# Performance work log

Measured on AMD Instinct MI355X. Metric: run time of the kernel, lower is better.

## Reference

```python
import jax, jax.numpy as jnp
import numpy as np
import math

D_MODEL = 2048
N_HEADS = 32
N_KV_HEADS = 8
HEAD_DIM = D_MODEL // N_HEADS  # 64
N_GROUPS = N_HEADS // N_KV_HEADS  # 4
MAX_SEQ_LEN = 2048
ROPE_THETA = 500000.0


def precompute_rope(head_dim, max_seq_len, theta=ROPE_THETA):
    freqs = 1.0 / theta ** (jnp.arange(0, head_dim, 2, dtype=jnp.float32) / head_dim)
    positions = jnp.arange(max_seq_len, dtype=jnp.float32)
    angles = jnp.outer(positions, freqs)  # [S, head_dim/2]
    return jnp.cos(angles), jnp.sin(angles)


def apply_rope(x, cos, sin):
    # x: [B, H, S, D]; cos/sin: [S, D/2]
    half = x.shape[-1] // 2
    x1, x2 = x[..., :half], x[..., half:]
    cos = cos[None, None]
    sin = sin[None, None]
    return jnp.concatenate([x1 * cos - x2 * sin, x1 * sin + x2 * cos], axis=-1)


def setup_inputs() -> dict:
    key = jax.random.key(0)
    k1, k2, k3, k4, k5 = jax.random.split(key, 5)
    B, S = 2, 2048
    x = jax.random.normal(k1, (B, S, D_MODEL), dtype=jnp.float32)
    sd = 1.0 / math.sqrt(D_MODEL)
    # weights stored as [in, out] so forward is x @ W (same math as torch Linear)
    W_q = jax.random.normal(k2, (D_MODEL, N_HEADS * HEAD_DIM), dtype=jnp.float32) * sd
    W_k = jax.random.normal(k3, (D_MODEL, N_KV_HEADS * HEAD_DIM), dtype=jnp.float32) * sd
    W_v = jax.random.normal(k4, (D_MODEL, N_KV_HEADS * HEAD_DIM), dtype=jnp.float32) * sd
    W_o = jax.random.normal(k5, (N_HEADS * HEAD_DIM, D_MODEL), dtype=jnp.float32) * sd
    cos, sin = precompute_rope(HEAD_DIM, MAX_SEQ_LEN)
    return {"x": x, "W_q": W_q, "W_k": W_k, "W_v": W_v, "W_o": W_o,
            "rope_cos": cos, "rope_sin": sin}


def reference(x, W_q, W_k, W_v, W_o, rope_cos, rope_sin):
    B, S, _ = x.shape
    scale = 1.0 / math.sqrt(HEAD_DIM)
    # projections -> [B, H, S, D]
    q = (x @ W_q).reshape(B, S, N_HEADS, HEAD_DIM).transpose(0, 2, 1, 3)
    k = (x @ W_k).reshape(B, S, N_KV_HEADS, HEAD_DIM).transpose(0, 2, 1, 3)
    v = (x @ W_v).reshape(B, S, N_KV_HEADS, HEAD_DIM).transpose(0, 2, 1, 3)
    # RoPE
    q = apply_rope(q, rope_cos[:S], rope_sin[:S])
    k = apply_rope(k, rope_cos[:S], rope_sin[:S])
    # GQA expand: repeat each KV head n_groups times
    k = jnp.repeat(k, N_GROUPS, axis=1)  # [B, H, S, D]
    v = jnp.repeat(v, N_GROUPS, axis=1)
    # scores + causal mask + softmax
    scores = jnp.einsum('bhqd,bhkd->bhqk', q, k) * scale
    causal = jnp.tril(jnp.ones((S, S), dtype=bool))
    scores = jnp.where(causal[None, None], scores, -jnp.inf)
    weights = jax.nn.softmax(scores, axis=-1)
    attn_out = jnp.einsum('bhqk,bhkd->bhqd', weights, v)
    out = attn_out.transpose(0, 2, 1, 3).reshape(B, S, N_HEADS * HEAD_DIM) @ W_o
    return out
```

## Files before the change

kernel.cpp:

```cpp
#include <hip/hip_runtime.h>
#include <hip/hip_bf16.h>

typedef __attribute__((ext_vector_type(8))) short short8;
typedef __attribute__((ext_vector_type(4))) short short4v;
typedef __attribute__((ext_vector_type(4))) float f32x4;

#define MFMA(A,B,C) __builtin_amdgcn_mfma_f32_16x16x32_bf16(A,B,C,0,0,0)
#define SW(row) ((((row) & 3)) | (((row) >> 1) & 4))
#define SCL 0.18033688f

__device__ __forceinline__ short f2bs(float f) {
    __hip_bfloat16 h = __float2bfloat16(f);
    union { __hip_bfloat16 h; short s; } u; u.h = h; return u.s;
}

__device__ __forceinline__ float exp2v(float x) {
    float r; asm("v_exp_f32 %0, %1" : "=v"(r) : "v"(x)); return r;
}

__device__ __forceinline__ unsigned cvtpk(float a, float b) {
    unsigned r; asm("v_cvt_pk_bf16_f32 %0, %1, %2" : "=v"(r) : "v"(a), "v"(b)); return r;
}

__device__ __forceinline__ void async16(void* lds, const void* g) {
    __builtin_amdgcn_global_load_lds(
        (const __attribute__((address_space(1))) unsigned int*)g,
        (__attribute__((address_space(3))) unsigned int*)lds, 16, 0, 0);
}

__global__ __launch_bounds__(256) void cast_bf16_k(const float* __restrict__ X,
                                                   short* __restrict__ Y, int n4) {
    int i = blockIdx.x * 256 + threadIdx.x;
    if (i >= n4) return;
    const float4 v = *(const float4*)(X + (size_t)i * 4);
    short4v o;
    o.x = f2bs(v.x); o.y = f2bs(v.y); o.z = f2bs(v.z); o.w = f2bs(v.w);
    *(short4v*)(Y + (size_t)i * 4) = o;
}

__global__ __launch_bounds__(256) void transpose_cast_k(const float* __restrict__ W,
                                                        short* __restrict__ Wt, int K, int N) {
    __shared__ float tile[32][33];
    int n0 = blockIdx.x * 32, k0 = blockIdx.y * 32;
    int tx = threadIdx.x, ty = threadIdx.y;
    #pragma unroll
    for (int i = 0; i < 32; i += 8)
        tile[ty + i][tx] = W[(size_t)(k0 + ty + i) * N + n0 + tx];
    __syncthreads();
    #pragma unroll
    for (int i = 0; i < 32; i += 8)
        Wt[(size_t)(n0 + ty + i) * K + k0 + tx] = f2bs(tile[tx][ty + i]);
}

__global__ __launch_bounds__(512, 2) void gemm_qkv_k(
    const short* __restrict__ A, const short* __restrict__ Bt,
    short* __restrict__ Cq, short* __restrict__ Ck, short* __restrict__ Cv,
    const float* __restrict__ rc, const float* __restrict__ rs,
    int M, int N, int K)
{
    extern __shared__ short lds[];
    const int t = threadIdx.x;
    const int l = t & 63, w = t >> 6;
    const int lo = l & 15, hi = l >> 4;
    const int wm = w >> 2, wn = w & 3;
    const int lr = l >> 3, ls = l & 7;

    const int nbx = gridDim.x;
    const int nwg = nbx * gridDim.y;
    const int bid0 = blockIdx.y * nbx + blockIdx.x;
    const int wg = (bid0 & 7) * (nwg >> 3) + (bid0 >> 3);
    const int tm = (wg % nbx) * 256, tn = (wg / nbx) * 256;

    const f32x4 z4 = {0.f, 0.f, 0.f, 0.f};
    f32x4 acc[8][4];
    #pragma unroll
    for (int m = 0; m < 8; ++m)
        #pragma unroll
        for (int n = 0; n < 4; ++n) acc[m][n] = z4;

    auto stage_half = [&](int kt, int buf, int h) {
        const size_t ko = (size_t)kt * 64;
        const short* src = (h < 2) ? A : Bt;
        const int rbase = (h == 1 || h == 3) ? 128 : 0;
        const int gbase = (h < 2) ? tm : tn;
        short* dst = lds + buf * 32768 + ((h < 2) ? 0 : 16384) + rbase * 64;
        #pragma unroll
        for (int j = 0; j < 2; ++j) {
            int g = w * 2 + j;
            int row = g * 8 + lr;
            int gs = ls ^ SW(row);
            async16(dst + g * 512, src + (size_t)(gbase + rbase + row) * K + ko + gs * 8);
        }
    };

    const int nkt = K >> 6;
    #pragma unroll
    for (int h = 0; h < 4; ++h) stage_half(0, 0, h);
    __syncthreads();

    int cur = 0;
    for (int kt = 0; kt < nkt; ++kt) {
        const bool pf = (kt + 1 < nkt);
        const short* Ab_ = lds + cur * 32768;
        const short* Bb_ = Ab_ + 16384;
        short8 af[4], bfr[4];
        #pragma unroll
        for (int ph = 0; ph < 4; ++ph) {
            const int ks = ph >> 1, mh = ph & 1;
            const int slot = ks * 4 + hi;
            #pragma unroll
            for (int mm = 0; mm < 4; ++mm) {
                int row = wm * 128 + (mh * 4 + mm) * 16 + lo;
                af[mm] = *(const short8*)(Ab_ + row * 64 + ((slot ^ SW(row)) << 3));
            }
            if (mh == 0) {
                #pragma unroll
                for (int n = 0; n < 4; ++n) {
                    int row = wn * 64 + n * 16 + lo;
                    bfr[n] = *(const short8*)(Bb_ + row * 64 + ((slot ^ SW(row)) << 3));
                }
            }
            if (pf && ph < 2) {
                stage_half(kt + 1, cur ^ 1, ph * 2);
                stage_half(kt + 1, cur ^ 1, ph * 2 + 1);
            }
            __builtin_amdgcn_s_barrier();
            asm volatile("s_waitcnt lgkmcnt(0)" ::: "memory");
            __builtin_amdgcn_sched_barrier(0);
            __builtin_amdgcn_s_setprio(1);
            #pragma unroll
            for (int n = 0; n < 4; ++n)
                #pragma unroll
                for (int mm = 0; mm < 4; ++mm)
                    acc[mh * 4 + mm][n] = MFMA(af[mm], bfr[n], acc[mh * 4 + mm][n]);
            __builtin_amdgcn_s_setprio(0);
            if (ph == 3 && pf)
                asm volatile("s_waitcnt vmcnt(0)" ::: "memory");
            __builtin_amdgcn_s_barrier();
        }
        cur ^= 1;
    }

    const int ctn = tn + wn * 64;
    if (ctn < 2048) {
        #pragma unroll
        for (int m = 0; m < 8; ++m)
            #pragma unroll
            for (int r = 0; r < 4; ++r) {
                int row = tm + wm * 128 + m * 16 + hi * 4 + r;
                int b = row >> 11, s = row & 2047;
                #pragma unroll
                for (int n = 0; n < 2; ++n) {
                    int col = ctn + n * 16 + lo;
                    int h = col >> 6, d = col & 63;
                    float x1 = acc[m][n][r], x2 = acc[m][n + 2][r];
                    float c = rc[s * 32 + d], sn = rs[s * 32 + d];
                    size_t base = (((size_t)b * 32 + h) * 2048 + s) * 64;
                    Cq[base + d]      = f2bs((x1 * c - x2 * sn) * SCL);
                    Cq[base + d + 32] = f2bs((x1 * sn + x2 * c) * SCL);
                }
            }
    } else if (ctn < 2560) {
        #pragma unroll
        for (int m = 0; m < 8; ++m)
            #pragma unroll
            for (int r = 0; r < 4; ++r) {
                int row = tm + wm * 128 + m * 16 + hi * 4 + r;
                int b = row >> 11, s = row & 2047;
                #pragma unroll
                for (int n = 0; n < 2; ++n) {
                    int col = ctn - 2048 + n * 16 + lo;
                    int h = col >> 6, d = col & 63;
                    float x1 = acc[m][n][r], x2 = acc[m][n + 2][r];
                    float c = rc[s * 32 + d], sn = rs[s * 32 + d];
                    size_t base = (((size_t)b * 8 + h) * 2048 + s) * 64;
                    Ck[base + d]      = f2bs(x1 * c - x2 * sn);
                    Ck[base + d + 32] = f2bs(x1 * sn + x2 * c);
                }
            }
    } else {
        #pragma unroll
        for (int m = 0; m < 8; ++m)
            #pragma unroll
            for (int r = 0; r < 4; ++r) {
                int row = tm + wm * 128 + m * 16 + hi * 4 + r;
                int b = row >> 11, s = row & 2047;
                #pragma unroll
                for (int n = 0; n < 4; ++n) {
                    int col = ctn - 2560 + n * 16 + lo;
                    int h = col >> 6, d = col & 63;
                    Cv[(((size_t)b * 8 + h) * 64 + d) * 2048 + s] = f2bs(acc[m][n][r]);
                }
            }
    }
}

__global__ __launch_bounds__(512, 2) void gemm_o_k(
    const short* __restrict__ A, const short* __restrict__ Bt,
    float* __restrict__ Cf, int M, int N, int K)
{
    extern __shared__ short lds[];
    const int t = threadIdx.x;
    const int l = t & 63, w = t >> 6;
    const int lo = l & 15, hi = l >> 4;
    const int wm = w >> 2, wn = w & 3;
    const int lr = l >> 3, ls = l & 7;

    const int nbx = gridDim.x;
    const int nwg = nbx * gridDim.y;
    const int bid0 = blockIdx.y * nbx + blockIdx.x;
    const int wg = (bid0 & 7) * (nwg >> 3) + (bid0 >> 3);
    const int tm = (wg % nbx) * 128, tn = (wg / nbx) * 256;

    const f32x4 z4 = {0.f, 0.f, 0.f, 0.f};
    f32x4 acc[4][4];
    #pragma unroll
    for (int m = 0; m < 4; ++m)
        #pragma unroll
        for (int n = 0; n < 4; ++n) acc[m][n] = z4;

    const int srow = w * 8 + lr;
    const int sswz = ls ^ SW(srow);

    auto stage_unit = [&](int kt, int buf, int u) {
        const size_t ko = (size_t)kt * 64;
        short* base = lds + buf * 24576;
        if (u < 2)
            async16(base + u * 4096 + w * 512,
                    A + (size_t)(tm + u * 64 + srow) * K + ko + sswz * 8);
        else
            async16(base + 8192 + (u - 2) * 4096 + w * 512,
                    Bt + (size_t)(tn + (u - 2) * 64 + srow) * K + ko + sswz * 8);
    };

    const int nkt = K >> 6;
    #pragma unroll
    for (int u = 0; u < 6; ++u) stage_unit(0, 0, u);
    #pragma unroll
    for (int u = 0; u < 6; ++u) stage_unit(1, 1, u);
    asm volatile("s_waitcnt vmcnt(6)" ::: "memory");
    __builtin_amdgcn_s_barrier();

    int cur = 0;
    for (int kt = 0; kt < nkt; ++kt) {
        int tgt = cur + 2; if (tgt >= 3) tgt -= 3;
        const bool pf2 = (kt + 2 < nkt);
        const bool pf1 = (kt + 1 < nkt);
        const short* Ab_ = lds + cur * 24576;
        const short* Bb_ = Ab_ + 8192;
        short8 af[4], bfr[4];
        #pragma unroll
        for (int ph = 0; ph < 2; ++ph) {
            const int slot = ph * 4 + hi;
            #pragma unroll
            for (int mm = 0; mm < 4; ++mm) {
                int row = wm * 64 + mm * 16 + lo;
                af[mm] = *(const short8*)(Ab_ + row * 64 + ((slot ^ SW(row)) << 3));
            }
            #pragma unroll
            for (int n = 0; n < 4; ++n) {
                int row = wn * 64 + n * 16 + lo;
                bfr[n] = *(const short8*)(Bb_ + row * 64 + ((slot ^ SW(row)) << 3));
            }
            if (pf2) {
                stage_unit(kt + 2, tgt, ph * 3);
                stage_unit(kt + 2, tgt, ph * 3 + 1);
                stage_unit(kt + 2, tgt, ph * 3 + 2);
            }
            __builtin_amdgcn_s_barrier();
            asm volatile("s_waitcnt lgkmcnt(0)" ::: "memory");
            __builtin_amdgcn_sched_barrier(0);
            __builtin_amdgcn_s_setprio(1);
            #pragma unroll
            for (int n = 0; n < 4; ++n)
                #pragma unroll
                for (int mm = 0; mm < 4; ++mm)
                    acc[mm][n] = MFMA(af[mm], bfr[n], acc[mm][n]);
            __builtin_amdgcn_s_setprio(0);
            if (ph == 1) {
                if (pf2)      asm volatile("s_waitcnt vmcnt(6)" ::: "memory");
                else if (pf1) asm volatile("s_waitcnt vmcnt(0)" ::: "memory");
            }
            __builtin_amdgcn_s_barrier();
        }
        cur = (cur == 2) ? 0 : cur + 1;
    }

    #pragma unroll
    for (int m = 0; m < 4; ++m)
        #pragma unroll
        for (int r = 0; r < 4; ++r) {
            int row = tm + wm * 64 + m * 16 + hi * 4 + r;
            #pragma unroll
            for (int n = 0; n < 4; ++n) {
                int col = tn + wn * 64 + n * 16 + lo;
                Cf[(size_t)row * N + col] = acc[m][n][r];
            }
        }
}

__global__ __launch_bounds__(256) void attn_k(
    const short* __restrict__ Qp, const short* __restrict__ Kp, const short* __restrict__ Vt,
    short* __restrict__ Ab)
{
    __shared__ short KV[2][8192];
    const int t = threadIdx.x, l = t & 63, w = t >> 6;
    const int lo = l & 15, hi = l >> 4;
    const int lr = l >> 3, ls = l & 7;
    const int pair = blockIdx.x;
    const int h = blockIdx.y, b = blockIdx.z;
    const int kvh = h >> 2;
    const size_t qbase  = (size_t)(b * 32 + h) * 2048 * 64;
    const size_t kbase  = (size_t)(b * 8 + kvh) * 2048 * 64;
    const size_t vtbase = (size_t)(b * 8 + kvh) * 64 * 2048;
    const size_t abase  = (size_t)b * 2048 * 2048 + (size_t)h * 64;

    for (int halfq = 0; halfq < 2; ++halfq) {
        const int qtile = halfq ? 31 - pair : pair;
        const int nkt = qtile + 1;

        short8 qf[2];
        {
            int qrow = qtile * 64 + w * 16 + lo;
            #pragma unroll
            for (int ks = 0; ks < 2; ++ks)
                qf[ks] = *(const short8*)(Qp + qbase + (size_t)qrow * 64 + (ks * 4 + hi) * 8);
        }

        const f32x4 z4 = {0.f, 0.f, 0.f, 0.f};
        float l_run = 0.f;
        f32x4 oacc[4];
        #pragma unroll
        for (int nd = 0; nd < 4; ++nd) oacc[nd] = z4;

        #pragma unroll
        for (int j = 0; j < 2; ++j) {
            int g8 = w * 2 + j;
            int row = g8 * 8 + lr;
            int gs = ls ^ SW(row);
            async16(&KV[0][g8 * 512],        Kp + kbase + (size_t)row * 64 + gs * 8);
            async16(&KV[0][4096 + g8 * 512], Vt + vtbase + (size_t)row * 2048 + gs * 8);
        }
        __syncthreads();

        int cur = 0;
        for (int kt = 0; kt < nkt; ++kt) {
            if (kt + 1 < nkt) {
                #pragma unroll
                for (int j = 0; j < 2; ++j) {
                    int g8 = w * 2 + j;
                    int row = g8 * 8 + lr;
                    int gs = ls ^ SW(row);
                    async16(&KV[cur ^ 1][g8 * 512],
                            Kp + kbase + (size_t)((kt + 1) * 64 + row) * 64 + gs * 8);
                    async16(&KV[cur ^ 1][4096 + g8 * 512],
                            Vt + vtbase + (size_t)row * 2048 + (kt + 1) * 64 + gs * 8);
                }
            }

            const short* Ks = &KV[cur][0];
            const short* Vs = &KV[cur][4096];

            f32x4 sacc[4];
            #pragma unroll
            for (int n = 0; n < 4; ++n) sacc[n] = z4;
            __builtin_amdgcn_s_setprio(1);
            #pragma unroll
            for (int ks = 0; ks < 2; ++ks) {
                const int slot = ks * 4 + hi;
                #pragma unroll
                for (int n = 0; n < 4; ++n) {
                    const int krow = ((lo >> 2) << 3) + ((n & 1) << 2) + (lo & 3) + ((n >> 1) << 5);
                    short8 kf = *(const short8*)(Ks + krow * 64 + ((slot ^ SW(krow)) << 3));
                    sacc[n] = MFMA(kf, qf[ks], sacc[n]);
                }
            }
            __builtin_amdgcn_s_setprio(0);

            float p[4][4];
            if (kt == qtile) {
                const int q = qtile * 64 + w * 16 + lo;
                #pragma unroll
                for (int n = 0; n < 4; ++n)
                    #pragma unroll
                    for (int r = 0; r < 4; ++r) {
                        int k = kt * 64 + hi * 8 + ((n & 1) << 2) + r + ((n >> 1) << 5);
                        p[n][r] = exp2v((k > q) ? -3e38f : sacc[n][r]);
                    }
            } else {
                #pragma unroll
                for (int n = 0; n < 4; ++n)
                    #pragma unroll
                    for (int r = 0; r < 4; ++r)
                        p[n][r] = exp2v(sacc[n][r]);
            }
            float rs0 = 0.f, rs1 = 0.f;
            #pragma unroll
            for (int n = 0; n < 4; ++n) {
                rs0 += p[n][0] + p[n][1];
                rs1 += p[n][2] + p[n][3];
            }
            l_run += rs0 + rs1;

            short8 afr[2];
            #pragma unroll
            for (int ks = 0; ks < 2; ++ks) {
                union { short8 s; unsigned u[4]; } pk;
                pk.u[0] = cvtpk(p[2 * ks][0],     p[2 * ks][1]);
                pk.u[1] = cvtpk(p[2 * ks][2],     p[2 * ks][3]);
                pk.u[2] = cvtpk(p[2 * ks + 1][0], p[2 * ks + 1][1]);
                pk.u[3] = cvtpk(p[2 * ks + 1][2], p[2 * ks + 1][3]);
                afr[ks] = pk.s;
            }

            __builtin_amdgcn_s_setprio(1);
            #pragma unroll
            for (int ks = 0; ks < 2; ++ks) {
                const int slot = ks * 4 + hi;
                #pragma unroll
                for (int nd = 0; nd < 4; ++nd) {
                    const int vrow = nd * 16 + lo;
                    short8 vf = *(const short8*)(Vs + vrow * 64 + ((slot ^ SW(vrow)) << 3));
                    oacc[nd] = MFMA(afr[ks], vf, oacc[nd]);
                }
            }
            __builtin_amdgcn_s_setprio(0);

            __syncthreads();
            cur ^= 1;
        }

        l_run += __shfl_xor(l_run, 16, 64);
        l_run += __shfl_xor(l_run, 32, 64);
        float rl[4];
        #pragma unroll
        for (int r = 0; r < 4; ++r)
            rl[r] = 1.0f / __shfl(l_run, (l & 48) | (hi * 4 + r), 64);
        #pragma unroll
        for (int nd = 0; nd < 4; ++nd)
            #pragma unroll
            for (int r = 0; r < 4; ++r) {
                int s = qtile * 64 + w * 16 + hi * 4 + r;
                Ab[abase + (size_t)s * 2048 + nd * 16 + lo] = f2bs(oacc[nd][r] * rl[r]);
            }
    }
}

extern "C" void kernel_launch(void* const* d_in, const int* in_sizes, int n_in,
                              void* d_out, int out_size, void* d_ws, size_t ws_size,
                              hipStream_t stream)
{
    const float* x  = (const float*)d_in[0];
    const float* Wq = (const float*)d_in[1];
    const float* Wk = (const float*)d_in[2];
    const float* Wv = (const float*)d_in[3];
    const float* Wo = (const float*)d_in[4];
    const float* rc = (const float*)d_in[5];
    const float* rs = (const float*)d_in[6];
    float* out = (float*)d_out;
    char* ws = (char*)d_ws;

    size_t off = 0;
    short* x_bf   = (short*)(ws + off); off += (size_t)4096 * 2048 * 2;
    short* Wqkv_t = (short*)(ws + off); off += (size_t)3072 * 2048 * 2;
    short* Wo_t   = (short*)(ws + off); off += (size_t)2048 * 2048 * 2;
    short* Qp     = (short*)(ws + off); off += (size_t)2 * 32 * 2048 * 64 * 2;
    short* Kp     = (short*)(ws + off); off += (size_t)2 * 8 * 2048 * 64 * 2;
    short* Vtb    = (short*)(ws + off); off += (size_t)2 * 8 * 64 * 2048 * 2;
    short* Ab     = (short*)(ws + off); off += (size_t)4096 * 2048 * 2;
    if (off > ws_size) return;

    const int LDS_QKV = 2 * 32768 * 2;
    const int LDS_O   = 3 * 24576 * 2;
    (void)hipFuncSetAttribute((const void*)gemm_qkv_k,
                              hipFuncAttributeMaxDynamicSharedMemorySize, LDS_QKV);
    (void)hipFuncSetAttribute((const void*)gemm_o_k,
                              hipFuncAttributeMaxDynamicSharedMemorySize, LDS_O);

    cast_bf16_k<<<8192, 256, 0, stream>>>(x, x_bf, 2097152);
    transpose_cast_k<<<dim3(64, 64), dim3(32, 8), 0, stream>>>(Wq, Wqkv_t, 2048, 2048);
    transpose_cast_k<<<dim3(16, 64), dim3(32, 8), 0, stream>>>(Wk, Wqkv_t + (size_t)2048 * 2048, 2048, 512);
    transpose_cast_k<<<dim3(16, 64), dim3(32, 8), 0, stream>>>(Wv, Wqkv_t + (size_t)2560 * 2048, 2048, 512);
    transpose_cast_k<<<dim3(64, 64), dim3(32, 8), 0, stream>>>(Wo, Wo_t, 2048, 2048);

    gemm_qkv_k<<<dim3(16, 12), 512, LDS_QKV, stream>>>(x_bf, Wqkv_t, Qp, Kp, Vtb,
                                                       rc, rs, 4096, 3072, 2048);

    attn_k<<<dim3(16, 32, 2), 256, 0, stream>>>(Qp, Kp, Vtb, Ab);

    gemm_o_k<<<dim3(32, 8), 512, LDS_O, stream>>>(Ab, Wo_t, out, 4096, 2048, 2048);
}
```

Before: 176.3 us.

## Share KV tiles across paired query tiles in attention and unify GEMM kernels

The attention kernel now processes both paired query tiles (pair and 31-pair) in a single pass over the key/value tiles. Each loaded KV tile feeds both query tiles, which halves KV loads for the shared prefix and interleaves independent MFMA chains. The QKV projection now reuses the 128x256 triple-buffered GEMM template that the output projection uses, with the RoPE/scatter epilogue chosen by a template parameter. That doubles the QKV grid, giving more workgroups for better load balance at the cost of reloading the weights more often. The attention change raises register pressure because it keeps two sets of accumulators and Q fragments.

```diff
diff --git a/kernel.cpp b/kernel.cpp
--- a/kernel.cpp
+++ b/kernel.cpp
@@ -52,152 +52,13 @@
         Wt[(size_t)(n0 + ty + i) * K + k0 + tx] = f2bs(tile[tx][ty + i]);
 }
 
-__global__ __launch_bounds__(512, 2) void gemm_qkv_k(
+template<int EPI>
+__global__ __launch_bounds__(512, 2) void gemm128_k(
     const short* __restrict__ A, const short* __restrict__ Bt,
-    short* __restrict__ Cq, short* __restrict__ Ck, short* __restrict__ Cv,
+    float* __restrict__ Cf, short* __restrict__ Cq, short* __restrict__ Ck,
+    short* __restrict__ Cv,
     const float* __restrict__ rc, const float* __restrict__ rs,
     int M, int N, int K)
-{
-    extern __shared__ short lds[];
-    const int t = threadIdx.x;
-    const int l = t & 63, w = t >> 6;
-    const int lo = l & 15, hi = l >> 4;
-    const int wm = w >> 2, wn = w & 3;
-    const int lr = l >> 3, ls = l & 7;
-
-    const int nbx = gridDim.x;
-    const int nwg = nbx * gridDim.y;
-    const int bid0 = blockIdx.y * nbx + blockIdx.x;
-    const int wg = (bid0 & 7) * (nwg >> 3) + (bid0 >> 3);
-    const int tm = (wg % nbx) * 256, tn = (wg / nbx) * 256;
-
-    const f32x4 z4 = {0.f, 0.f, 0.f, 0.f};
-    f32x4 acc[8][4];
-    #pragma unroll
-    for (int m = 0; m < 8; ++m)
-        #pragma unroll
-        for (int n = 0; n < 4; ++n) acc[m][n] = z4;
-
-    auto stage_half = [&](int kt, int buf, int h) {
-        const size_t ko = (size_t)kt * 64;
-        const short* src = (h < 2) ? A : Bt;
-        const int rbase = (h == 1 || h == 3) ? 128 : 0;
-        const int gbase = (h < 2) ? tm : tn;
-        short* dst = lds + buf * 32768 + ((h < 2) ? 0 : 16384) + rbase * 64;
-        #pragma unroll
-        for (int j = 0; j < 2; ++j) {
-            int g = w * 2 + j;
-            int row = g * 8 + lr;
-            int gs = ls ^ SW(row);
-            async16(dst + g * 512, src + (size_t)(gbase + rbase + row) * K + ko + gs * 8);
-        }
-    };
-
-    const int nkt = K >> 6;
-    #pragma unroll
-    for (int h = 0; h < 4; ++h) stage_half(0, 0, h);
-    __syncthreads();
-
-    int cur = 0;
-    for (int kt = 0; kt < nkt; ++kt) {
-        const bool pf = (kt + 1 < nkt);
-        const short* Ab_ = lds + cur * 32768;
-        const short* Bb_ = Ab_ + 16384;
-        short8 af[4], bfr[4];
-        #pragma unroll
-        for (int ph = 0; ph < 4; ++ph) {
-            const int ks = ph >> 1, mh = ph & 1;
-            const int slot = ks * 4 + hi;
-            #pragma unroll
-            for (int mm = 0; mm < 4; ++mm) {
-                int row = wm * 128 + (mh * 4 + mm) * 16 + lo;
-                af[mm] = *(const short8*)(Ab_ + row * 64 + ((slot ^ SW(row)) << 3));
-            }
-            if (mh == 0) {
-                #pragma unroll
-                for (int n = 0; n < 4; ++n) {
-                    int row = wn * 64 + n * 16 + lo;
-                    bfr[n] = *(const short8*)(Bb_ + row * 64 + ((slot ^ SW(row)) << 3));
-                }
-            }
-            if (pf && ph < 2) {
-                stage_half(kt + 1, cur ^ 1, ph * 2);
-                stage_half(kt + 1, cur ^ 1, ph * 2 + 1);
-            }
-            __builtin_amdgcn_s_barrier();
-            asm volatile("s_waitcnt lgkmcnt(0)" ::: "memory");
-            __builtin_amdgcn_sched_barrier(0);
-            __builtin_amdgcn_s_setprio(1);
-            #pragma unroll
-            for (int n = 0; n < 4; ++n)
-                #pragma unroll
-                for (int mm = 0; mm < 4; ++mm)
-                    acc[mh * 4 + mm][n] = MFMA(af[mm], bfr[n], acc[mh * 4 + mm][n]);
-            __builtin_amdgcn_s_setprio(0);
-            if (ph == 3 && pf)
-                asm volatile("s_waitcnt vmcnt(0)" ::: "memory");
-            __builtin_amdgcn_s_barrier();
-        }
-        cur ^= 1;
-    }
-
-    const int ctn = tn + wn * 64;
-    if (ctn < 2048) {
-        #pragma unroll
-        for (int m = 0; m < 8; ++m)
-            #pragma unroll
-            for (int r = 0; r < 4; ++r) {
-                int row = tm + wm * 128 + m * 16 + hi * 4 + r;
-                int b = row >> 11, s = row & 2047;
-                #pragma unroll
-                for (int n = 0; n < 2; ++n) {
-                    int col = ctn + n * 16 + lo;
-                    int h = col >> 6, d = col & 63;
-                    float x1 = acc[m][n][r], x2 = acc[m][n + 2][r];
-                    float c = rc[s * 32 + d], sn = rs[s * 32 + d];
-                    size_t base = (((size_t)b * 32 + h) * 2048 + s) * 64;
-                    Cq[base + d]      = f2bs((x1 * c - x2 * sn) * SCL);
-                    Cq[base + d + 32] = f2bs((x1 * sn + x2 * c) * SCL);
-                }
-            }
-    } else if (ctn < 2560) {
-        #pragma unroll
-        for (int m = 0; m < 8; ++m)
-            #pragma unroll
-            for (int r = 0; r < 4; ++r) {
-                int row = tm + wm * 128 + m * 16 + hi * 4 + r;
-                int b = row >> 11, s = row & 2047;
-                #pragma unroll
-                for (int n = 0; n < 2; ++n) {
-                    int col = ctn - 2048 + n * 16 + lo;
-                    int h = col >> 6, d = col & 63;
-                    float x1 = acc[m][n][r], x2 = acc[m][n + 2][r];
-                    float c = rc[s * 32 + d], sn = rs[s * 32 + d];
-                    size_t base = (((size_t)b * 8 + h) * 2048 + s) * 64;
-                    Ck[base + d]      = f2bs(x1 * c - x2 * sn);
-                    Ck[base + d + 32] = f2bs(x1 * sn + x2 * c);
-                }
-            }
-    } else {
-        #pragma unroll
-        for (int m = 0; m < 8; ++m)
-            #pragma unroll
-            for (int r = 0; r < 4; ++r) {
-                int row = tm + wm * 128 + m * 16 + hi * 4 + r;
-                int b = row >> 11, s = row & 2047;
-                #pragma unroll
-                for (int n = 0; n < 4; ++n) {
-                    int col = ctn - 2560 + n * 16 + lo;
-                    int h = col >> 6, d = col & 63;
-                    Cv[(((size_t)b * 8 + h) * 64 + d) * 2048 + s] = f2bs(acc[m][n][r]);
-                }
-            }
-    }
-}
-
-__global__ __launch_bounds__(512, 2) void gemm_o_k(
-    const short* __restrict__ A, const short* __restrict__ Bt,
-    float* __restrict__ Cf, int M, int N, int K)
 {
     extern __shared__ short lds[];
     const int t = threadIdx.x;
@@ -286,17 +147,72 @@
         cur = (cur == 2) ? 0 : cur + 1;
     }
 
-    #pragma unroll
-    for (int m = 0; m < 4; ++m)
-        #pragma unroll
-        for (int r = 0; r < 4; ++r) {
-            int row = tm + wm * 64 + m * 16 + hi * 4 + r;
-            #pragma unroll
-            for (int n = 0; n < 4; ++n) {
-                int col = tn + wn * 64 + n * 16 + lo;
-                Cf[(size_t)row * N + col] = acc[m][n][r];
-            }
-        }
+    if constexpr (EPI == 0) {
+        #pragma unroll
+        for (int m = 0; m < 4; ++m)
+            #pragma unroll
+            for (int r = 0; r < 4; ++r) {
+                int row = tm + wm * 64 + m * 16 + hi * 4 + r;
+                #pragma unroll
+                for (int n = 0; n < 4; ++n) {
+                    int col = tn + wn * 64 + n * 16 + lo;
+                    Cf[(size_t)row * N + col] = acc[m][n][r];
+                }
+            }
+    } else {
+        const int ctn = tn + wn * 64;
+        if (ctn < 2048) {
+            #pragma unroll
+            for (int m = 0; m < 4; ++m)
+                #pragma unroll
+                for (int r = 0; r < 4; ++r) {
+                    int row = tm + wm * 64 + m * 16 + hi * 4 + r;
+                    int b = row >> 11, s = row & 2047;
+                    #pragma unroll
+                    for (int n = 0; n < 2; ++n) {
+                        int col = ctn + n * 16 + lo;
+                        int h = col >> 6, d = col & 63;
+                        float x1 = acc[m][n][r], x2 = acc[m][n + 2][r];
+                        float c = rc[s * 32 + d], sn = rs[s * 32 + d];
+                        size_t base = (((size_t)b * 32 + h) * 2048 + s) * 64;
+                        Cq[base + d]      = f2bs((x1 * c - x2 * sn) * SCL);
+                        Cq[base + d + 32] = f2bs((x1 * sn + x2 * c) * SCL);
+                    }
+                }
+        } else if (ctn < 2560) {
+            #pragma unroll
+            for (int m = 0; m < 4; ++m)
+                #pragma unroll
+                for (int r = 0; r < 4; ++r) {
+                    int row = tm + wm * 64 + m * 16 + hi * 4 + r;
+                    int b = row >> 11, s = row & 2047;
+                    #pragma unroll
+                    for (int n = 0; n < 2; ++n) {
+                        int col = ctn - 2048 + n * 16 + lo;
+                        int h = col >> 6, d = col & 63;
+                        float x1 = acc[m][n][r], x2 = acc[m][n + 2][r];
+                        float c = rc[s * 32 + d], sn = rs[s * 32 + d];
+                        size_t base = (((size_t)b * 8 + h) * 2048 + s) * 64;
+                        Ck[base + d]      = f2bs(x1 * c - x2 * sn);
+                        Ck[base + d + 32] = f2bs(x1 * sn + x2 * c);
+                    }
+                }
+        } else {
+            #pragma unroll
+            for (int m = 0; m < 4; ++m)
+                #pragma unroll
+                for (int r = 0; r < 4; ++r) {
+                    int row = tm + wm * 64 + m * 16 + hi * 4 + r;
+                    int b = row >> 11, s = row & 2047;
+                    #pragma unroll
+                    for (int n = 0; n < 4; ++n) {
+                        int col = ctn - 2560 + n * 16 + lo;
+                        int h = col >> 6, d = col & 63;
+                        Cv[(((size_t)b * 8 + h) * 64 + d) * 2048 + s] = f2bs(acc[m][n][r]);
+                    }
+                }
+        }
+    }
 }
 
 __global__ __launch_bounds__(256) void attn_k(
@@ -315,56 +231,95 @@
     const size_t vtbase = (size_t)(b * 8 + kvh) * 64 * 2048;
     const size_t abase  = (size_t)b * 2048 * 2048 + (size_t)h * 64;
 
-    for (int halfq = 0; halfq < 2; ++halfq) {
-        const int qtile = halfq ? 31 - pair : pair;
-        const int nkt = qtile + 1;
-
-        short8 qf[2];
-        {
-            int qrow = qtile * 64 + w * 16 + lo;
-            #pragma unroll
-            for (int ks = 0; ks < 2; ++ks)
-                qf[ks] = *(const short8*)(Qp + qbase + (size_t)qrow * 64 + (ks * 4 + hi) * 8);
-        }
-
-        const f32x4 z4 = {0.f, 0.f, 0.f, 0.f};
-        float l_run = 0.f;
-        f32x4 oacc[4];
-        #pragma unroll
-        for (int nd = 0; nd < 4; ++nd) oacc[nd] = z4;
-
-        #pragma unroll
-        for (int j = 0; j < 2; ++j) {
-            int g8 = w * 2 + j;
-            int row = g8 * 8 + lr;
-            int gs = ls ^ SW(row);
-            async16(&KV[0][g8 * 512],        Kp + kbase + (size_t)row * 64 + gs * 8);
-            async16(&KV[0][4096 + g8 * 512], Vt + vtbase + (size_t)row * 2048 + gs * 8);
-        }
-        __syncthreads();
-
-        int cur = 0;
-        for (int kt = 0; kt < nkt; ++kt) {
-            if (kt + 1 < nkt) {
-                #pragma unroll
-                for (int j = 0; j < 2; ++j) {
-                    int g8 = w * 2 + j;
-                    int row = g8 * 8 + lr;
-                    int gs = ls ^ SW(row);
-                    async16(&KV[cur ^ 1][g8 * 512],
-                            Kp + kbase + (size_t)((kt + 1) * 64 + row) * 64 + gs * 8);
-                    async16(&KV[cur ^ 1][4096 + g8 * 512],
-                            Vt + vtbase + (size_t)row * 2048 + (kt + 1) * 64 + gs * 8);
-                }
-            }
-
-            const short* Ks = &KV[cur][0];
-            const short* Vs = &KV[cur][4096];
-
-            f32x4 sacc[4];
-            #pragma unroll
-            for (int n = 0; n < 4; ++n) sacc[n] = z4;
-            __builtin_amdgcn_s_setprio(1);
+    const int qtA = pair, qtB = 31 - pair;
+    const int nkt = qtB + 1;
+
+    short8 qfA[2], qfB[2];
+    {
+        int qrA = qtA * 64 + w * 16 + lo;
+        int qrB = qtB * 64 + w * 16 + lo;
+        #pragma unroll
+        for (int ks = 0; ks < 2; ++ks) {
+            qfA[ks] = *(const short8*)(Qp + qbase + (size_t)qrA * 64 + (ks * 4 + hi) * 8);
+            qfB[ks] = *(const short8*)(Qp + qbase + (size_t)qrB * 64 + (ks * 4 + hi) * 8);
+        }
+    }
+
+    const f32x4 z4 = {0.f, 0.f, 0.f, 0.f};
+    float lA = 0.f, lB = 0.f;
+    f32x4 oA[4], oB[4];
+    #pragma unroll
+    for (int nd = 0; nd < 4; ++nd) { oA[nd] = z4; oB[nd] = z4; }
+
+    auto softmax_pack = [&](f32x4 (&s)[4], int qt, int kt, float& lrun, short8 (&afr)[2]) {
+        float p[4][4];
+        if (kt == qt) {
+            const int q = qt * 64 + w * 16 + lo;
+            #pragma unroll
+            for (int n = 0; n < 4; ++n)
+                #pragma unroll
+                for (int r = 0; r < 4; ++r) {
+                    int k = kt * 64 + hi * 8 + ((n & 1) << 2) + r + ((n >> 1) << 5);
+                    p[n][r] = exp2v((k > q) ? -3e38f : s[n][r]);
+                }
+        } else {
+            #pragma unroll
+            for (int n = 0; n < 4; ++n)
+                #pragma unroll
+                for (int r = 0; r < 4; ++r)
+                    p[n][r] = exp2v(s[n][r]);
+        }
+        float acc = 0.f;
+        #pragma unroll
+        for (int n = 0; n < 4; ++n)
+            #pragma unroll
+            for (int r = 0; r < 4; ++r) acc += p[n][r];
+        lrun += acc;
+        #pragma unroll
+        for (int ks = 0; ks < 2; ++ks) {
+            union { short8 s8; unsigned u[4]; } pk;
+            pk.u[0] = cvtpk(p[2 * ks][0],     p[2 * ks][1]);
+            pk.u[1] = cvtpk(p[2 * ks][2],     p[2 * ks][3]);
+            pk.u[2] = cvtpk(p[2 * ks + 1][0], p[2 * ks + 1][1]);
+            pk.u[3] = cvtpk(p[2 * ks + 1][2], p[2 * ks + 1][3]);
+            afr[ks] = pk.s8;
+        }
+    };
+
+    #pragma unroll
+    for (int j = 0; j < 2; ++j) {
+        int g8 = w * 2 + j;
+        int row = g8 * 8 + lr;
+        int gs = ls ^ SW(row);
+        async16(&KV[0][g8 * 512],        Kp + kbase + (size_t)row * 64 + gs * 8);
+        async16(&KV[0][4096 + g8 * 512], Vt + vtbase + (size_t)row * 2048 + gs * 8);
+    }
+    __syncthreads();
+
+    int cur = 0;
+    for (int kt = 0; kt < nkt; ++kt) {
+        const bool doA = (kt <= qtA);
+        if (kt + 1 < nkt) {
+            #pragma unroll
+            for (int j = 0; j < 2; ++j) {
+                int g8 = w * 2 + j;
+                int row = g8 * 8 + lr;
+                int gs = ls ^ SW(row);
+                async16(&KV[cur ^ 1][g8 * 512],
+                        Kp + kbase + (size_t)((kt + 1) * 64 + row) * 64 + gs * 8);
+                async16(&KV[cur ^ 1][4096 + g8 * 512],
+                        Vt + vtbase + (size_t)row * 2048 + (kt + 1) * 64 + gs * 8);
+            }
+        }
+
+        const short* Ks = &KV[cur][0];
+        const short* Vs = &KV[cur][4096];
+
+        f32x4 sA[4], sB[4];
+        #pragma unroll
+        for (int n = 0; n < 4; ++n) { sA[n] = z4; sB[n] = z4; }
+        __builtin_amdgcn_s_setprio(1);
+        if (doA) {
             #pragma unroll
             for (int ks = 0; ks < 2; ++ks) {
                 const int slot = ks * 4 + hi;
@@ -372,48 +327,30 @@
                 for (int n = 0; n < 4; ++n) {
                     const int krow = ((lo >> 2) << 3) + ((n & 1) << 2) + (lo & 3) + ((n >> 1) << 5);
                     short8 kf = *(const short8*)(Ks + krow * 64 + ((slot ^ SW(krow)) << 3));
-                    sacc[n] = MFMA(kf, qf[ks], sacc[n]);
-                }
-            }
-            __builtin_amdgcn_s_setprio(0);
-
-            float p[4][4];
-            if (kt == qtile) {
-                const int q = qtile * 64 + w * 16 + lo;
-                #pragma unroll
-                for (int n = 0; n < 4; ++n)
-                    #pragma unroll
-                    for (int r = 0; r < 4; ++r) {
-                        int k = kt * 64 + hi * 8 + ((n & 1) << 2) + r + ((n >> 1) << 5);
-                        p[n][r] = exp2v((k > q) ? -3e38f : sacc[n][r]);
-                    }
-            } else {
-                #pragma unroll
-                for (int n = 0; n < 4; ++n)
-                    #pragma unroll
-                    for (int r = 0; r < 4; ++r)
-                        p[n][r] = exp2v(sacc[n][r]);
-            }
-            float rs0 = 0.f, rs1 = 0.f;
-            #pragma unroll
-            for (int n = 0; n < 4; ++n) {
-                rs0 += p[n][0] + p[n][1];
-                rs1 += p[n][2] + p[n][3];
-            }
-            l_run += rs0 + rs1;
-
-            short8 afr[2];
+                    sB[n] = MFMA(kf, qfB[ks], sB[n]);
+                    sA[n] = MFMA(kf, qfA[ks], sA[n]);
+                }
+            }
+        } else {
             #pragma unroll
             for (int ks = 0; ks < 2; ++ks) {
-                union { short8 s; unsigned u[4]; } pk;
-                pk.u[0] = cvtpk(p[2 * ks][0],     p[2 * ks][1]);
-                pk.u[1] = cvtpk(p[2 * ks][2],     p[2 * ks][3]);
-                pk.u[2] = cvtpk(p[2 * ks + 1][0], p[2 * ks + 1][1]);
-                pk.u[3] = cvtpk(p[2 * ks + 1][2], p[2 * ks + 1][3]);
-                afr[ks] = pk.s;
-            }
-
-            __builtin_amdgcn_s_setprio(1);
+                const int slot = ks * 4 + hi;
+                #pragma unroll
+                for (int n = 0; n < 4; ++n) {
+                    const int krow = ((lo >> 2) << 3) + ((n & 1) << 2) + (lo & 3) + ((n >> 1) << 5);
+                    short8 kf = *(const short8*)(Ks + krow * 64 + ((slot ^ SW(krow)) << 3));
+                    sB[n] = MFMA(kf, qfB[ks], sB[n]);
+                }
+            }
+        }
+        __builtin_amdgcn_s_setprio(0);
+
+        short8 afrA[2], afrB[2];
+        softmax_pack(sB, qtB, kt, lB, afrB);
+        if (doA) softmax_pack(sA, qtA, kt, lA, afrA);
+
+        __builtin_amdgcn_s_setprio(1);
+        if (doA) {
             #pragma unroll
             for (int ks = 0; ks < 2; ++ks) {
                 const int slot = ks * 4 + hi;
@@ -421,29 +358,45 @@
                 for (int nd = 0; nd < 4; ++nd) {
                     const int vrow = nd * 16 + lo;
                     short8 vf = *(const short8*)(Vs + vrow * 64 + ((slot ^ SW(vrow)) << 3));
-                    oacc[nd] = MFMA(afr[ks], vf, oacc[nd]);
-                }
-            }
-            __builtin_amdgcn_s_setprio(0);
-
-            __syncthreads();
-            cur ^= 1;
-        }
-
-        l_run += __shfl_xor(l_run, 16, 64);
-        l_run += __shfl_xor(l_run, 32, 64);
+                    oB[nd] = MFMA(afrB[ks], vf, oB[nd]);
+                    oA[nd] = MFMA(afrA[ks], vf, oA[nd]);
+                }
+            }
+        } else {
+            #pragma unroll
+            for (int ks = 0; ks < 2; ++ks) {
+                const int slot = ks * 4 + hi;
+                #pragma unroll
+                for (int nd = 0; nd < 4; ++nd) {
+                    const int vrow = nd * 16 + lo;
+                    short8 vf = *(const short8*)(Vs + vrow * 64 + ((slot ^ SW(vrow)) << 3));
+                    oB[nd] = MFMA(afrB[ks], vf, oB[nd]);
+                }
+            }
+        }
+        __builtin_amdgcn_s_setprio(0);
+
+        __syncthreads();
+        cur ^= 1;
+    }
+
+    auto epilogue = [&](int qt, float lrun, f32x4 (&o)[4]) {
+        lrun += __shfl_xor(lrun, 16, 64);
+        lrun += __shfl_xor(lrun, 32, 64);
         float rl[4];
         #pragma unroll
         for (int r = 0; r < 4; ++r)
-            rl[r] = 1.0f / __shfl(l_run, (l & 48) | (hi * 4 + r), 64);
+            rl[r] = 1.0f / __shfl(lrun, (l & 48) | (hi * 4 + r), 64);
         #pragma unroll
         for (int nd = 0; nd < 4; ++nd)
             #pragma unroll
             for (int r = 0; r < 4; ++r) {
-                int s = qtile * 64 + w * 16 + hi * 4 + r;
-                Ab[abase + (size_t)s * 2048 + nd * 16 + lo] = f2bs(oacc[nd][r] * rl[r]);
-            }
-    }
+                int s = qt * 64 + w * 16 + hi * 4 + r;
+                Ab[abase + (size_t)s * 2048 + nd * 16 + lo] = f2bs(o[nd][r] * rl[r]);
+            }
+    };
+    epilogue(qtB, lB, oB);
+    epilogue(qtA, lA, oA);
 }
 
 extern "C" void kernel_launch(void* const* d_in, const int* in_sizes, int n_in,
@@ -470,12 +423,11 @@
     short* Ab     = (short*)(ws + off); off += (size_t)4096 * 2048 * 2;
     if (off > ws_size) return;
 
-    const int LDS_QKV = 2 * 32768 * 2;
-    const int LDS_O   = 3 * 24576 * 2;
-    (void)hipFuncSetAttribute((const void*)gemm_qkv_k,
-                              hipFuncAttributeMaxDynamicSharedMemorySize, LDS_QKV);
-    (void)hipFuncSetAttribute((const void*)gemm_o_k,
-                              hipFuncAttributeMaxDynamicSharedMemorySize, LDS_O);
+    const int LDS_G = 3 * 24576 * 2;
+    (void)hipFuncSetAttribute((const void*)gemm128_k<4>,
+                              hipFuncAttributeMaxDynamicSharedMemorySize, LDS_G);
+    (void)hipFuncSetAttribute((const void*)gemm128_k<0>,
+                              hipFuncAttributeMaxDynamicSharedMemorySize, LDS_G);
 
     cast_bf16_k<<<8192, 256, 0, stream>>>(x, x_bf, 2097152);
     transpose_cast_k<<<dim3(64, 64), dim3(32, 8), 0, stream>>>(Wq, Wqkv_t, 2048, 2048);
@@ -483,10 +435,11 @@
     transpose_cast_k<<<dim3(16, 64), dim3(32, 8), 0, stream>>>(Wv, Wqkv_t + (size_t)2560 * 2048, 2048, 512);
     transpose_cast_k<<<dim3(64, 64), dim3(32, 8), 0, stream>>>(Wo, Wo_t, 2048, 2048);
 
-    gemm_qkv_k<<<dim3(16, 12), 512, LDS_QKV, stream>>>(x_bf, Wqkv_t, Qp, Kp, Vtb,
+    gemm128_k<4><<<dim3(32, 12), 512, LDS_G, stream>>>(x_bf, Wqkv_t, nullptr, Qp, Kp, Vtb,
                                                        rc, rs, 4096, 3072, 2048);
 
     attn_k<<<dim3(16, 32, 2), 256, 0, stream>>>(Qp, Kp, Vtb, Ab);
 
-    gemm_o_k<<<dim3(32, 8), 512, LDS_O, stream>>>(Ab, Wo_t, out, 4096, 2048, 2048);
-}
+    gemm128_k<0><<<dim3(32, 8), 512, LDS_G, stream>>>(Ab, Wo_t, out, nullptr, nullptr, nullptr,
+                                                      nullptr, nullptr, 4096, 2048, 2048);
+}
```

Measured after the change: 199.9 us. +13.4%, slower.

## Shrink QKV GEMM tile and switch to triple-buffered K-depth-32 pipeline

Applied to the files above, without the earlier changes.

The QKV projection GEMM goes from 256x256 tiles with K-step 64 and double buffering to 128x256 tiles with K-step 32 and a three-stage LDS ring that prefetches two steps ahead. The swizzle is adapted to 32-wide rows, and launch bounds are raised to allow more blocks per CU. The grid doubles to 384 blocks, which improves CU coverage and latency hiding on a 256-CU part. In exchange each block does less MFMA work per operand load, so arithmetic intensity drops and there are more barriers per unit of work.

```diff
diff --git a/kernel.cpp b/kernel.cpp
--- a/kernel.cpp
+++ b/kernel.cpp
@@ -7,6 +7,7 @@
 
 #define MFMA(A,B,C) __builtin_amdgcn_mfma_f32_16x16x32_bf16(A,B,C,0,0,0)
 #define SW(row) ((((row) & 3)) | (((row) >> 1) & 4))
+#define SW32(row) ((((row) & 3)) ^ (((row) >> 2) & 3))
 #define SCL 0.18033688f
 
 __device__ __forceinline__ short f2bs(float f) {
@@ -52,7 +53,7 @@
         Wt[(size_t)(n0 + ty + i) * K + k0 + tx] = f2bs(tile[tx][ty + i]);
 }
 
-__global__ __launch_bounds__(512, 2) void gemm_qkv_k(
+__global__ __launch_bounds__(512, 4) void gemm_qkv_k(
     const short* __restrict__ A, const short* __restrict__ Bt,
     short* __restrict__ Cq, short* __restrict__ Ck, short* __restrict__ Cv,
     const float* __restrict__ rc, const float* __restrict__ rs,
@@ -63,91 +64,86 @@
     const int l = t & 63, w = t >> 6;
     const int lo = l & 15, hi = l >> 4;
     const int wm = w >> 2, wn = w & 3;
-    const int lr = l >> 3, ls = l & 7;
 
     const int nbx = gridDim.x;
     const int nwg = nbx * gridDim.y;
     const int bid0 = blockIdx.y * nbx + blockIdx.x;
     const int wg = (bid0 & 7) * (nwg >> 3) + (bid0 >> 3);
-    const int tm = (wg % nbx) * 256, tn = (wg / nbx) * 256;
+    const int tm = (wg % nbx) * 128, tn = (wg / nbx) * 256;
 
     const f32x4 z4 = {0.f, 0.f, 0.f, 0.f};
-    f32x4 acc[8][4];
-    #pragma unroll
-    for (int m = 0; m < 8; ++m)
+    f32x4 acc[4][4];
+    #pragma unroll
+    for (int m = 0; m < 4; ++m)
         #pragma unroll
         for (int n = 0; n < 4; ++n) acc[m][n] = z4;
 
-    auto stage_half = [&](int kt, int buf, int h) {
-        const size_t ko = (size_t)kt * 64;
-        const short* src = (h < 2) ? A : Bt;
-        const int rbase = (h == 1 || h == 3) ? 128 : 0;
-        const int gbase = (h < 2) ? tm : tn;
-        short* dst = lds + buf * 32768 + ((h < 2) ? 0 : 16384) + rbase * 64;
-        #pragma unroll
-        for (int j = 0; j < 2; ++j) {
-            int g = w * 2 + j;
-            int row = g * 8 + lr;
-            int gs = ls ^ SW(row);
-            async16(dst + g * 512, src + (size_t)(gbase + rbase + row) * K + ko + gs * 8);
-        }
+    const int srow = t >> 2;
+    const int scol = (t & 3) ^ SW32(srow);
+
+    auto stage_unit = [&](int kt, int buf, int u) {
+        const size_t ko = (size_t)kt * 32;
+        short* dst = lds + buf * 12288 + u * 4096 + w * 512;
+        if (u == 0)
+            async16(dst, A + (size_t)(tm + srow) * K + ko + scol * 8);
+        else
+            async16(dst, Bt + (size_t)(tn + (u - 1) * 128 + srow) * K + ko + scol * 8);
     };
 
-    const int nkt = K >> 6;
-    #pragma unroll
-    for (int h = 0; h < 4; ++h) stage_half(0, 0, h);
-    __syncthreads();
+    const int nkt = K >> 5;
+    #pragma unroll
+    for (int u = 0; u < 3; ++u) stage_unit(0, 0, u);
+    #pragma unroll
+    for (int u = 0; u < 3; ++u) stage_unit(1, 1, u);
+    asm volatile("s_waitcnt vmcnt(3)" ::: "memory");
+    __builtin_amdgcn_s_barrier();
 
     int cur = 0;
     for (int kt = 0; kt < nkt; ++kt) {
-        const bool pf = (kt + 1 < nkt);
-        const short* Ab_ = lds + cur * 32768;
-        const short* Bb_ = Ab_ + 16384;
+        int tgt = cur + 2; if (tgt >= 3) tgt -= 3;
+        const bool pf2 = (kt + 2 < nkt);
+        const bool pf1 = (kt + 1 < nkt);
+        const short* Ab_ = lds + cur * 12288;
+        const short* Bb_ = Ab_ + 4096;
         short8 af[4], bfr[4];
         #pragma unroll
-        for (int ph = 0; ph < 4; ++ph) {
-            const int ks = ph >> 1, mh = ph & 1;
-            const int slot = ks * 4 + hi;
-            #pragma unroll
-            for (int mm = 0; mm < 4; ++mm) {
-                int row = wm * 128 + (mh * 4 + mm) * 16 + lo;
-                af[mm] = *(const short8*)(Ab_ + row * 64 + ((slot ^ SW(row)) << 3));
-            }
-            if (mh == 0) {
-                #pragma unroll
-                for (int n = 0; n < 4; ++n) {
-                    int row = wn * 64 + n * 16 + lo;
-                    bfr[n] = *(const short8*)(Bb_ + row * 64 + ((slot ^ SW(row)) << 3));
-                }
-            }
-            if (pf && ph < 2) {
-                stage_half(kt + 1, cur ^ 1, ph * 2);
-                stage_half(kt + 1, cur ^ 1, ph * 2 + 1);
-            }
-            __builtin_amdgcn_s_barrier();
-            asm volatile("s_waitcnt lgkmcnt(0)" ::: "memory");
-            __builtin_amdgcn_sched_barrier(0);
-            __builtin_amdgcn_s_setprio(1);
-            #pragma unroll
-            for (int n = 0; n < 4; ++n)
-                #pragma unroll
-                for (int mm = 0; mm < 4; ++mm)
-                    acc[mh * 4 + mm][n] = MFMA(af[mm], bfr[n], acc[mh * 4 + mm][n]);
-            __builtin_amdgcn_s_setprio(0);
-            if (ph == 3 && pf)
-                asm volatile("s_waitcnt vmcnt(0)" ::: "memory");
-            __builtin_amdgcn_s_barrier();
-        }
-        cur ^= 1;
+        for (int mm = 0; mm < 4; ++mm) {
+            int row = wm * 64 + mm * 16 + lo;
+            af[mm] = *(const short8*)(Ab_ + row * 32 + ((hi ^ SW32(row)) << 3));
+        }
+        #pragma unroll
+        for (int n = 0; n < 4; ++n) {
+            int row = wn * 64 + n * 16 + lo;
+            bfr[n] = *(const short8*)(Bb_ + row * 32 + ((hi ^ SW32(row)) << 3));
+        }
+        if (pf2) {
+            stage_unit(kt + 2, tgt, 0);
+            stage_unit(kt + 2, tgt, 1);
+            stage_unit(kt + 2, tgt, 2);
+        }
+        __builtin_amdgcn_s_barrier();
+        asm volatile("s_waitcnt lgkmcnt(0)" ::: "memory");
+        __builtin_amdgcn_sched_barrier(0);
+        __builtin_amdgcn_s_setprio(1);
+        #pragma unroll
+        for (int n = 0; n < 4; ++n)
+            #pragma unroll
+            for (int mm = 0; mm < 4; ++mm)
+                acc[mm][n] = MFMA(af[mm], bfr[n], acc[mm][n]);
+        __builtin_amdgcn_s_setprio(0);
+        if (pf2)      asm volatile("s_waitcnt vmcnt(3)" ::: "memory");
+        else if (pf1) asm volatile("s_waitcnt vmcnt(0)" ::: "memory");
+        __builtin_amdgcn_s_barrier();
+        cur = (cur == 2) ? 0 : cur + 1;
     }
 
     const int ctn = tn + wn * 64;
     if (ctn < 2048) {
         #pragma unroll
-        for (int m = 0; m < 8; ++m)
+        for (int m = 0; m < 4; ++m)
             #pragma unroll
             for (int r = 0; r < 4; ++r) {
-                int row = tm + wm * 128 + m * 16 + hi * 4 + r;
+                int row = tm + wm * 64 + m * 16 + hi * 4 + r;
                 int b = row >> 11, s = row & 2047;
                 #pragma unroll
                 for (int n = 0; n < 2; ++n) {
@@ -162,10 +158,10 @@
             }
     } else if (ctn < 2560) {
         #pragma unroll
-        for (int m = 0; m < 8; ++m)
+        for (int m = 0; m < 4; ++m)
             #pragma unroll
             for (int r = 0; r < 4; ++r) {
-                int row = tm + wm * 128 + m * 16 + hi * 4 + r;
+                int row = tm + wm * 64 + m * 16 + hi * 4 + r;
                 int b = row >> 11, s = row & 2047;
                 #pragma unroll
                 for (int n = 0; n < 2; ++n) {
@@ -180,10 +176,10 @@
             }
     } else {
         #pragma unroll
-        for (int m = 0; m < 8; ++m)
+        for (int m = 0; m < 4; ++m)
             #pragma unroll
             for (int r = 0; r < 4; ++r) {
-                int row = tm + wm * 128 + m * 16 + hi * 4 + r;
+                int row = tm + wm * 64 + m * 16 + hi * 4 + r;
                 int b = row >> 11, s = row & 2047;
                 #pragma unroll
                 for (int n = 0; n < 4; ++n) {
@@ -470,7 +466,7 @@
     short* Ab     = (short*)(ws + off); off += (size_t)4096 * 2048 * 2;
     if (off > ws_size) return;
 
-    const int LDS_QKV = 2 * 32768 * 2;
+    const int LDS_QKV = 3 * 12288 * 2;
     const int LDS_O   = 3 * 24576 * 2;
     (void)hipFuncSetAttribute((const void*)gemm_qkv_k,
                               hipFuncAttributeMaxDynamicSharedMemorySize, LDS_QKV);
@@ -483,7 +479,7 @@
     transpose_cast_k<<<dim3(16, 64), dim3(32, 8), 0, stream>>>(Wv, Wqkv_t + (size_t)2560 * 2048, 2048, 512);
     transpose_cast_k<<<dim3(64, 64), dim3(32, 8), 0, stream>>>(Wo, Wo_t, 2048, 2048);
 
-    gemm_qkv_k<<<dim3(16, 12), 512, LDS_QKV, stream>>>(x_bf, Wqkv_t, Qp, Kp, Vtb,
+    gemm_qkv_k<<<dim3(32, 12), 512, LDS_QKV, stream>>>(x_bf, Wqkv_t, Qp, Kp, Vtb,
                                                        rc, rs, 4096, 3072, 2048);
 
     attn_k<<<dim3(16, 32, 2), 256, 0, stream>>>(Qp, Kp, Vtb, Ab);
```

After: 183.5 us. 4.1% more time.
